# Performance work log

Measured on AMD Instinct MI355X. Metric: run time of the kernel, lower is better.

## Reference

```python
import jax, jax.numpy as jnp
import numpy as np

B, N, D, H = 8, 2048, 768, 64

def setup_inputs() -> dict:
    key = jax.random.key(0)
    k1, k2, k3, k4 = jax.random.split(key, 4)
    return {
        "input": jax.random.normal(k1, (B, N, D), dtype=jnp.float32),
        "Wq": jax.random.normal(k2, (D, H), dtype=jnp.float32) * (D ** -0.5),
        "Wk": jax.random.normal(k3, (D, H), dtype=jnp.float32) * (D ** -0.5),
        "Wv": jax.random.normal(k4, (D, H), dtype=jnp.float32) * (D ** -0.5),
    }

def reference(input, Wq, Wk, Wv):
    # Projections: [B, N, H]
    Q = jnp.einsum('bnd,dh->bnh', input, Wq)
    K = jnp.einsum('bnd,dh->bnh', input, Wk)
    V = jnp.einsum('bnd,dh->bnh', input, Wv)
    # Raw scores [B, N, N]; mask BEFORE scaling (as in original; -inf/scale == -inf)
    scores = jnp.einsum('bqh,bkh->bqk', Q, K)
    n = input.shape[1]
    causal = jnp.tril(jnp.ones((n, n), dtype=bool))
    scores = jnp.where(causal, scores, -jnp.inf)
    scores = scores / (K.shape[-1] ** 0.5)
    attn = jax.nn.softmax(scores, axis=-1)
    # dropout_rate=0 -> identity (eval mode)
    return jnp.einsum('bqk,bkh->bqh', attn, V)
```

## Files before the change

kernel.cpp:

```cpp
#include <hip/hip_runtime.h>
#include <stdint.h>

typedef __bf16 bf16_t;
typedef __bf16 bf16x8 __attribute__((ext_vector_type(8)));
typedef float floatx4 __attribute__((ext_vector_type(4)));

#define B_ 8
#define N_ 2048
#define D_ 768
#define H_ 64

__device__ __forceinline__ bf16_t f2bf(float f) {
    union { float f; uint32_t u; } v; v.f = f;
    uint32_t u = v.u;
    uint32_t r = (u + 0x7fffu + ((u >> 16) & 1u)) >> 16;
    union { unsigned short s; bf16_t b; } o; o.s = (unsigned short)r;
    return o.b;
}

__device__ __forceinline__ void async_cp16(void* l, const void* g) {
    __builtin_amdgcn_global_load_lds(
        (const __attribute__((address_space(1))) uint32_t*)g,
        (__attribute__((address_space(3))) uint32_t*)l, 16, 0, 0);
}

__global__ void wt_kernel(const float* __restrict__ Wq,
                          const float* __restrict__ Wk,
                          const float* __restrict__ Wv,
                          bf16_t* __restrict__ Wt) {
    const int h = threadIdx.x;
    const int k = blockIdx.x;
    const int s = blockIdx.y;
    const float* W = (s == 0) ? Wq : (s == 1) ? Wk : Wv;
    float v = W[k * H_ + h];
    if (s == 0) v *= 0.125f * 1.4426950408889634f;
    Wt[(size_t)(s * 64 + h) * D_ + k] = f2bf(v);
}

__launch_bounds__(256, 2)
__global__ void proj_kernel(const float* __restrict__ X,
                            const bf16_t* __restrict__ Wt,
                            bf16_t* __restrict__ Qb,
                            bf16_t* __restrict__ Kb,
                            bf16_t* __restrict__ Vt) {
    const int wave = threadIdx.x >> 6;
    const int lane = threadIdx.x & 63;
    const int quad = lane >> 4;
    const int l16  = lane & 15;
    const int rowhalf = wave & 1;
    const int colhalf = wave >> 1;
    const int m0blk = blockIdx.x * 32;

    __shared__ __align__(16) float  As[2][32 * 64];
    __shared__ __align__(16) bf16_t Bs[2][192 * 64];

    floatx4 acc[6];
#pragma unroll
    for (int i = 0; i < 6; i++) acc[i] = (floatx4){0.f, 0.f, 0.f, 0.f};

    auto stage = [&](int buf, int k0) {
#pragma unroll
        for (int i = 0; i < 2; i++) {
            const int r = (wave * 2 + i) * 4 + (lane >> 4);
            const int c = (lane & 15) ^ (r & 15);
            const float* g = X + (size_t)(m0blk + r) * D_ + k0 + c * 4;
            async_cp16((char*)&As[buf][0] + (wave * 2 + i) * 1024, g);
        }
#pragma unroll
        for (int i = 0; i < 6; i++) {
            const int r = (wave * 6 + i) * 8 + (lane >> 3);
            const int c = (lane & 7) ^ (r & 7);
            const bf16_t* g = Wt + (size_t)r * D_ + k0 + c * 8;
            async_cp16((char*)&Bs[buf][0] + (wave * 6 + i) * 1024, g);
        }
    };

    const int arow = rowhalf * 16 + l16;

    stage(0, 0);
    for (int ch = 0; ch < 12; ch++) {
        __syncthreads();
        if (ch + 1 < 12) stage((ch + 1) & 1, (ch + 1) * 64);

        const char* Ab = (const char*)&As[ch & 1][0];
        const char* Bb = (const char*)&Bs[ch & 1][0];
#pragma unroll
        for (int kh = 0; kh < 2; kh++) {
            const int c0 = kh * 8 + quad * 2;
            float4 xa = *(const float4*)(Ab + arow * 256 + ((c0 ^ l16) & 15) * 16);
            float4 xb = *(const float4*)(Ab + arow * 256 + (((c0 + 1) ^ l16) & 15) * 16);
            bf16x8 af;
            af[0] = f2bf(xa.x); af[1] = f2bf(xa.y);
            af[2] = f2bf(xa.z); af[3] = f2bf(xa.w);
            af[4] = f2bf(xb.x); af[5] = f2bf(xb.y);
            af[6] = f2bf(xb.z); af[7] = f2bf(xb.w);
            const int cb = kh * 4 + quad;
#pragma unroll
            for (int nt = 0; nt < 6; nt++) {
                const int n = colhalf * 96 + nt * 16 + l16;
                bf16x8 bf = *(const bf16x8*)(Bb + n * 128 + ((cb ^ (n & 7))) * 16);
                acc[nt] = __builtin_amdgcn_mfma_f32_16x16x32_bf16(af, bf, acc[nt], 0, 0, 0);
            }
        }
    }

#pragma unroll
    for (int nt = 0; nt < 6; nt++) {
        const int c = colhalf * 96 + nt * 16 + l16;
#pragma unroll
        for (int r = 0; r < 4; r++) {
            const int m = m0blk + rowhalf * 16 + quad * 4 + r;
            bf16_t val = f2bf(acc[nt][r]);
            if (c < 64) {
                Qb[(size_t)m * H_ + c] = val;
            } else if (c < 128) {
                Kb[(size_t)m * H_ + (c - 64)] = val;
            } else {
                const int b = m >> 11, n = m & 2047, h = c - 128;
                Vt[((size_t)b * H_ + h) * N_ + n] = val;
            }
        }
    }
}

__launch_bounds__(256, 4)
__global__ void attn_kernel(const bf16_t* __restrict__ Qb,
                            const bf16_t* __restrict__ Kb,
                            const bf16_t* __restrict__ Vt,
                            float* __restrict__ Out) {
    const int x = blockIdx.x;
    const int b = blockIdx.y;
    const int z = blockIdx.z;
    const int qt = z ? (127 - x) : x;
    const int q0 = qt * 16;

    const int wave = threadIdx.x >> 6;
    const int lane = threadIdx.x & 63;
    const int quad = lane >> 4;
    const int l16  = lane & 15;

    const bf16_t* Qp = Qb + ((size_t)b * N_ + q0) * H_;
    const bf16_t* Kp = Kb + (size_t)b * N_ * H_;
    const bf16_t* Vp = Vt + (size_t)b * H_ * N_;

    bf16x8 qf0 = *(const bf16x8*)(Qp + (size_t)l16 * H_ + quad * 8);
    bf16x8 qf1 = *(const bf16x8*)(Qp + (size_t)l16 * H_ + 32 + quad * 8);

    bf16x8 ones;
    {
        bf16_t one = f2bf(1.0f);
#pragma unroll
        for (int i = 0; i < 8; i++) ones[i] = one;
    }

    floatx4 o[4];
#pragma unroll
    for (int i = 0; i < 4; i++) o[i] = (floatx4){0.f, 0.f, 0.f, 0.f};
    floatx4 lsum = (floatx4){0.f, 0.f, 0.f, 0.f};

    __shared__ __align__(16) bf16_t Pl[4][16][32];
    __shared__ float Ol[3][16][64];
    __shared__ float Ll[3][16];

    const int kt_max = q0 >> 5;

    for (int kt = wave; kt <= kt_max; kt += 4) {
        const int k0 = kt << 5;

        const bf16_t* kp0 = Kp + (size_t)(k0 + l16) * H_ + quad * 8;
        const bf16_t* kp1 = kp0 + 16 * H_;
        bf16x8 kfa = *(const bf16x8*)kp0;
        bf16x8 kfb = *(const bf16x8*)(kp0 + 32);
        bf16x8 kfc = *(const bf16x8*)kp1;
        bf16x8 kfd = *(const bf16x8*)(kp1 + 32);
        const bf16_t* vp = Vp + (size_t)l16 * N_ + k0 + quad * 8;
        bf16x8 vf0 = *(const bf16x8*)(vp);
        bf16x8 vf1 = *(const bf16x8*)(vp + (size_t)16 * N_);
        bf16x8 vf2 = *(const bf16x8*)(vp + (size_t)32 * N_);
        bf16x8 vf3 = *(const bf16x8*)(vp + (size_t)48 * N_);

        floatx4 s0 = (floatx4){0.f, 0.f, 0.f, 0.f};
        floatx4 s1 = (floatx4){0.f, 0.f, 0.f, 0.f};
        s0 = __builtin_amdgcn_mfma_f32_16x16x32_bf16(qf0, kfa, s0, 0, 0, 0);
        s0 = __builtin_amdgcn_mfma_f32_16x16x32_bf16(qf1, kfb, s0, 0, 0, 0);
        s1 = __builtin_amdgcn_mfma_f32_16x16x32_bf16(qf0, kfc, s1, 0, 0, 0);
        s1 = __builtin_amdgcn_mfma_f32_16x16x32_bf16(qf1, kfd, s1, 0, 0, 0);

        float p[8];
        if (k0 + 31 <= q0) {
#pragma unroll
            for (int r = 0; r < 4; r++) {
                p[r]     = exp2f(s0[r]);
                p[4 + r] = exp2f(s1[r]);
            }
        } else {
            const int qrow = q0 + quad * 4;
#pragma unroll
            for (int r = 0; r < 4; r++) {
                p[r]     = (k0 + l16      <= qrow + r) ? exp2f(s0[r]) : 0.f;
                p[4 + r] = (k0 + 16 + l16 <= qrow + r) ? exp2f(s1[r]) : 0.f;
            }
        }

#pragma unroll
        for (int r = 0; r < 4; r++) {
            Pl[wave][quad * 4 + r][l16]      = f2bf(p[r]);
            Pl[wave][quad * 4 + r][16 + l16] = f2bf(p[4 + r]);
        }
        bf16x8 pf = *(const bf16x8*)(&Pl[wave][l16][quad * 8]);

        lsum = __builtin_amdgcn_mfma_f32_16x16x32_bf16(pf, ones, lsum, 0, 0, 0);
        o[0] = __builtin_amdgcn_mfma_f32_16x16x32_bf16(pf, vf0, o[0], 0, 0, 0);
        o[1] = __builtin_amdgcn_mfma_f32_16x16x32_bf16(pf, vf1, o[1], 0, 0, 0);
        o[2] = __builtin_amdgcn_mfma_f32_16x16x32_bf16(pf, vf2, o[2], 0, 0, 0);
        o[3] = __builtin_amdgcn_mfma_f32_16x16x32_bf16(pf, vf3, o[3], 0, 0, 0);
    }

    __syncthreads();
    if (wave != 0) {
#pragma unroll
        for (int nt = 0; nt < 4; nt++)
#pragma unroll
            for (int r = 0; r < 4; r++)
                Ol[wave - 1][quad * 4 + r][nt * 16 + l16] = o[nt][r];
        if (l16 == 0) {
#pragma unroll
            for (int r = 0; r < 4; r++)
                Ll[wave - 1][quad * 4 + r] = lsum[r];
        }
    }
    __syncthreads();
    if (wave == 0) {
#pragma unroll
        for (int r = 0; r < 4; r++) {
            const int row = quad * 4 + r;
            float l = lsum[r] + Ll[0][row] + Ll[1][row] + Ll[2][row];
            float inv = 1.0f / l;
#pragma unroll
            for (int nt = 0; nt < 4; nt++) {
                const int col = nt * 16 + l16;
                float v = o[nt][r] + Ol[0][row][col] + Ol[1][row][col] + Ol[2][row][col];
                Out[((size_t)b * N_ + q0 + row) * H_ + col] = v * inv;
            }
        }
    }
}

extern "C" void kernel_launch(void* const* d_in, const int* in_sizes, int n_in,
                              void* d_out, int out_size, void* d_ws, size_t ws_size,
                              hipStream_t stream) {
    const float* X  = (const float*)d_in[0];
    const float* Wq = (const float*)d_in[1];
    const float* Wk = (const float*)d_in[2];
    const float* Wv = (const float*)d_in[3];
    float* Out = (float*)d_out;

    char* ws = (char*)d_ws;
    bf16_t* Qb = (bf16_t*)(ws);
    bf16_t* Kb = (bf16_t*)(ws + (size_t)(2u << 20));
    bf16_t* Vt = (bf16_t*)(ws + (size_t)(4u << 20));
    bf16_t* Wt = (bf16_t*)(ws + (size_t)(6u << 20));

    hipLaunchKernelGGL(wt_kernel, dim3(768, 3), dim3(64), 0, stream, Wq, Wk, Wv, Wt);
    hipLaunchKernelGGL(proj_kernel, dim3(512), dim3(256), 0, stream, X, Wt, Qb, Kb, Vt);
    hipLaunchKernelGGL(attn_kernel, dim3(64, 8, 2), dim3(256), 0, stream, Qb, Kb, Vt, Out);
}
```

Before: 133.1 us.

## Double-buffer K/V tiles in LDS via async global-to-LDS loads per wave

Each wave now prefetches its K and V tiles into a private double-buffered LDS region using async global_load_lds copies with an XOR swizzle. Manual waitcnt and sched_barriers overlap the next tile's load with the current tile's MFMA work, replacing direct register loads from global memory. The P scratch buffer gets a padded row stride, and the output-reduction buffers alias the staging memory. LDS use grows to about 72KB per block, so launch bounds drop to 2 blocks per SM and occupancy is reduced.

```diff
diff --git a/kernel.cpp b/kernel.cpp
--- a/kernel.cpp
+++ b/kernel.cpp
@@ -9,6 +9,10 @@
 #define N_ 2048
 #define D_ 768
 #define H_ 64
+
+#define WAIT_VM8()   { __builtin_amdgcn_sched_barrier(0); __builtin_amdgcn_s_waitcnt(0x0F78); __builtin_amdgcn_sched_barrier(0); }
+#define WAIT_VM0()   { __builtin_amdgcn_sched_barrier(0); __builtin_amdgcn_s_waitcnt(0x0F70); __builtin_amdgcn_sched_barrier(0); }
+#define WAIT_LGKM0() { __builtin_amdgcn_sched_barrier(0); __builtin_amdgcn_s_waitcnt(0xC07F); __builtin_amdgcn_sched_barrier(0); }
 
 __device__ __forceinline__ bf16_t f2bf(float f) {
     union { float f; uint32_t u; } v; v.f = f;
@@ -123,7 +127,7 @@
     }
 }
 
-__launch_bounds__(256, 4)
+__launch_bounds__(256, 2)
 __global__ void attn_kernel(const bf16_t* __restrict__ Qb,
                             const bf16_t* __restrict__ Kb,
                             const bf16_t* __restrict__ Vt,
@@ -139,9 +143,15 @@
     const int quad = lane >> 4;
     const int l16  = lane & 15;
 
+    __shared__ __align__(16) char smem[4 * 16384 + 4 * 16 * 56 * 2];
+    char* stg = smem;
+    bf16_t* Pl = (bf16_t*)(smem + 65536);
+    float* Ol  = (float*)smem;
+    float* Ll  = (float*)(smem + 12288);
+
     const bf16_t* Qp = Qb + ((size_t)b * N_ + q0) * H_;
-    const bf16_t* Kp = Kb + (size_t)b * N_ * H_;
-    const bf16_t* Vp = Vt + (size_t)b * H_ * N_;
+    const char* Kp = (const char*)(Kb + (size_t)b * N_ * H_);
+    const char* Vp = (const char*)(Vt + (size_t)b * H_ * N_);
 
     bf16x8 qf0 = *(const bf16x8*)(Qp + (size_t)l16 * H_ + quad * 8);
     bf16x8 qf1 = *(const bf16x8*)(Qp + (size_t)l16 * H_ + 32 + quad * 8);
@@ -158,26 +168,50 @@
     for (int i = 0; i < 4; i++) o[i] = (floatx4){0.f, 0.f, 0.f, 0.f};
     floatx4 lsum = (floatx4){0.f, 0.f, 0.f, 0.f};
 
-    __shared__ __align__(16) bf16_t Pl[4][16][32];
-    __shared__ float Ol[3][16][64];
-    __shared__ float Ll[3][16];
-
-    const int kt_max = q0 >> 5;
-
-    for (int kt = wave; kt <= kt_max; kt += 4) {
+    char* mybase = stg + wave * 16384;
+
+    const int rK = lane >> 3, cK = lane & 7;
+    const int rV = lane >> 2, cV = lane & 3;
+    auto stage_kv = [&](int k0, char* buf) {
+#pragma unroll
+        for (int i = 0; i < 4; i++) {
+            const int r = i * 8 + rK;
+            const char* g = Kp + (size_t)(k0 + r) * 128 + (cK ^ (r & 7)) * 16;
+            async_cp16(buf + i * 1024, g);
+        }
+#pragma unroll
+        for (int i = 0; i < 4; i++) {
+            const int r = i * 16 + rV;
+            const char* g = Vp + (size_t)r * 4096 + (size_t)k0 * 2 + (cV ^ (r & 3)) * 16;
+            async_cp16(buf + 4096 + i * 1024, g);
+        }
+    };
+
+    const int ktm = q0 >> 5;
+
+    if (wave <= ktm)     stage_kv(wave << 5,       mybase);
+    if (wave + 4 <= ktm) stage_kv((wave + 4) << 5, mybase + 8192);
+
+    for (int kt = wave; kt <= ktm; kt += 4) {
         const int k0 = kt << 5;
-
-        const bf16_t* kp0 = Kp + (size_t)(k0 + l16) * H_ + quad * 8;
-        const bf16_t* kp1 = kp0 + 16 * H_;
-        bf16x8 kfa = *(const bf16x8*)kp0;
-        bf16x8 kfb = *(const bf16x8*)(kp0 + 32);
-        bf16x8 kfc = *(const bf16x8*)kp1;
-        bf16x8 kfd = *(const bf16x8*)(kp1 + 32);
-        const bf16_t* vp = Vp + (size_t)l16 * N_ + k0 + quad * 8;
-        bf16x8 vf0 = *(const bf16x8*)(vp);
-        bf16x8 vf1 = *(const bf16x8*)(vp + (size_t)16 * N_);
-        bf16x8 vf2 = *(const bf16x8*)(vp + (size_t)32 * N_);
-        bf16x8 vf3 = *(const bf16x8*)(vp + (size_t)48 * N_);
+        const int buf = (((kt - wave) >> 2) & 1);
+        const char* kb = mybase + buf * 8192;
+        const char* vb = kb + 4096;
+
+        if (kt + 4 <= ktm) { WAIT_VM8(); } else { WAIT_VM0(); }
+
+        const int krow = l16 * 128;
+        bf16x8 kfa = *(const bf16x8*)(kb + krow        + ((quad    ) ^ (l16 & 7)) * 16);
+        bf16x8 kfb = *(const bf16x8*)(kb + krow        + ((quad + 4) ^ (l16 & 7)) * 16);
+        bf16x8 kfc = *(const bf16x8*)(kb + krow + 2048 + ((quad    ) ^ (l16 & 7)) * 16);
+        bf16x8 kfd = *(const bf16x8*)(kb + krow + 2048 + ((quad + 4) ^ (l16 & 7)) * 16);
+        bf16x8 vf0 = *(const bf16x8*)(vb + (l16     ) * 64 + (quad ^ (l16 & 3)) * 16);
+        bf16x8 vf1 = *(const bf16x8*)(vb + (l16 + 16) * 64 + (quad ^ (l16 & 3)) * 16);
+        bf16x8 vf2 = *(const bf16x8*)(vb + (l16 + 32) * 64 + (quad ^ (l16 & 3)) * 16);
+        bf16x8 vf3 = *(const bf16x8*)(vb + (l16 + 48) * 64 + (quad ^ (l16 & 3)) * 16);
+
+        WAIT_LGKM0();
+        if (kt + 8 <= ktm) stage_kv((kt + 8) << 5, mybase + buf * 8192);
 
         floatx4 s0 = (floatx4){0.f, 0.f, 0.f, 0.f};
         floatx4 s1 = (floatx4){0.f, 0.f, 0.f, 0.f};
@@ -202,12 +236,13 @@
             }
         }
 
+        bf16_t* Pw = Pl + wave * 16 * 56;
 #pragma unroll
         for (int r = 0; r < 4; r++) {
-            Pl[wave][quad * 4 + r][l16]      = f2bf(p[r]);
-            Pl[wave][quad * 4 + r][16 + l16] = f2bf(p[4 + r]);
-        }
-        bf16x8 pf = *(const bf16x8*)(&Pl[wave][l16][quad * 8]);
+            Pw[(quad * 4 + r) * 56 + l16]      = f2bf(p[r]);
+            Pw[(quad * 4 + r) * 56 + 16 + l16] = f2bf(p[4 + r]);
+        }
+        bf16x8 pf = *(const bf16x8*)(Pw + l16 * 56 + quad * 8);
 
         lsum = __builtin_amdgcn_mfma_f32_16x16x32_bf16(pf, ones, lsum, 0, 0, 0);
         o[0] = __builtin_amdgcn_mfma_f32_16x16x32_bf16(pf, vf0, o[0], 0, 0, 0);
@@ -218,15 +253,16 @@
 
     __syncthreads();
     if (wave != 0) {
+        float* Ow = Ol + (wave - 1) * 16 * 64;
 #pragma unroll
         for (int nt = 0; nt < 4; nt++)
 #pragma unroll
             for (int r = 0; r < 4; r++)
-                Ol[wave - 1][quad * 4 + r][nt * 16 + l16] = o[nt][r];
+                Ow[(quad * 4 + r) * 64 + nt * 16 + l16] = o[nt][r];
         if (l16 == 0) {
 #pragma unroll
             for (int r = 0; r < 4; r++)
-                Ll[wave - 1][quad * 4 + r] = lsum[r];
+                Ll[(wave - 1) * 16 + quad * 4 + r] = lsum[r];
         }
     }
     __syncthreads();
@@ -234,12 +270,13 @@
 #pragma unroll
         for (int r = 0; r < 4; r++) {
             const int row = quad * 4 + r;
-            float l = lsum[r] + Ll[0][row] + Ll[1][row] + Ll[2][row];
+            float l = lsum[r] + Ll[row] + Ll[16 + row] + Ll[32 + row];
             float inv = 1.0f / l;
 #pragma unroll
             for (int nt = 0; nt < 4; nt++) {
                 const int col = nt * 16 + l16;
-                float v = o[nt][r] + Ol[0][row][col] + Ol[1][row][col] + Ol[2][row][col];
+                float v = o[nt][r] + Ol[row * 64 + col]
+                        + Ol[(16 + row) * 64 + col] + Ol[(32 + row) * 64 + col];
                 Out[((size_t)b * N_ + q0 + row) * H_ + col] = v * inv;
             }
         }
```

Measured after the change: 126.1 us. -5.2%, faster.

## Restructure attention kernel to 32-row query tiles with async double-buffered LDS K/V staging

Applied to the files above, without the earlier changes.

The attention kernel now handles 32 query rows per block using 32x32x16 MFMAs, which halves the grid and doubles K/V reuse per load. Each wave streams K and V tiles into its own swizzled LDS double buffer through async global-to-LDS copies, with explicit waitcnt barriers, so loads overlap compute. The row sum is now accumulated in registers instead of through an MFMA against a ones vector. In exchange it uses more LDS and registers (launch bounds drop to 2) and has fewer blocks, which may hurt occupancy and load balance.

```diff
diff --git a/kernel.cpp b/kernel.cpp
--- a/kernel.cpp
+++ b/kernel.cpp
@@ -2,13 +2,19 @@
 #include <stdint.h>
 
 typedef __bf16 bf16_t;
+typedef __bf16 bf16x4 __attribute__((ext_vector_type(4)));
 typedef __bf16 bf16x8 __attribute__((ext_vector_type(8)));
 typedef float floatx4 __attribute__((ext_vector_type(4)));
+typedef float floatx16 __attribute__((ext_vector_type(16)));
 
 #define B_ 8
 #define N_ 2048
 #define D_ 768
 #define H_ 64
+
+#define WAIT_VM8()   { __builtin_amdgcn_sched_barrier(0); __builtin_amdgcn_s_waitcnt(0x0F78); __builtin_amdgcn_sched_barrier(0); }
+#define WAIT_VM0()   { __builtin_amdgcn_sched_barrier(0); __builtin_amdgcn_s_waitcnt(0x0F70); __builtin_amdgcn_sched_barrier(0); }
+#define WAIT_LGKM0() { __builtin_amdgcn_sched_barrier(0); __builtin_amdgcn_s_waitcnt(0xC07F); __builtin_amdgcn_sched_barrier(0); }
 
 __device__ __forceinline__ bf16_t f2bf(float f) {
     union { float f; uint32_t u; } v; v.f = f;
@@ -123,7 +129,7 @@
     }
 }
 
-__launch_bounds__(256, 4)
+__launch_bounds__(256, 2)
 __global__ void attn_kernel(const bf16_t* __restrict__ Qb,
                             const bf16_t* __restrict__ Kb,
                             const bf16_t* __restrict__ Vt,
@@ -131,117 +137,150 @@
     const int x = blockIdx.x;
     const int b = blockIdx.y;
     const int z = blockIdx.z;
-    const int qt = z ? (127 - x) : x;
-    const int q0 = qt * 16;
+    const int qt = z ? (63 - x) : x;
+    const int q0 = qt * 32;
 
     const int wave = threadIdx.x >> 6;
     const int lane = threadIdx.x & 63;
-    const int quad = lane >> 4;
-    const int l16  = lane & 15;
-
-    const bf16_t* Qp = Qb + ((size_t)b * N_ + q0) * H_;
-    const bf16_t* Kp = Kb + (size_t)b * N_ * H_;
-    const bf16_t* Vp = Vt + (size_t)b * H_ * N_;
-
-    bf16x8 qf0 = *(const bf16x8*)(Qp + (size_t)l16 * H_ + quad * 8);
-    bf16x8 qf1 = *(const bf16x8*)(Qp + (size_t)l16 * H_ + 32 + quad * 8);
-
-    bf16x8 ones;
-    {
-        bf16_t one = f2bf(1.0f);
-#pragma unroll
-        for (int i = 0; i < 8; i++) ones[i] = one;
-    }
-
-    floatx4 o[4];
-#pragma unroll
-    for (int i = 0; i < 4; i++) o[i] = (floatx4){0.f, 0.f, 0.f, 0.f};
-    floatx4 lsum = (floatx4){0.f, 0.f, 0.f, 0.f};
-
-    __shared__ __align__(16) bf16_t Pl[4][16][32];
-    __shared__ float Ol[3][16][64];
-    __shared__ float Ll[3][16];
-
-    const int kt_max = q0 >> 5;
-
-    for (int kt = wave; kt <= kt_max; kt += 4) {
-        const int k0 = kt << 5;
-
-        const bf16_t* kp0 = Kp + (size_t)(k0 + l16) * H_ + quad * 8;
-        const bf16_t* kp1 = kp0 + 16 * H_;
-        bf16x8 kfa = *(const bf16x8*)kp0;
-        bf16x8 kfb = *(const bf16x8*)(kp0 + 32);
-        bf16x8 kfc = *(const bf16x8*)kp1;
-        bf16x8 kfd = *(const bf16x8*)(kp1 + 32);
-        const bf16_t* vp = Vp + (size_t)l16 * N_ + k0 + quad * 8;
-        bf16x8 vf0 = *(const bf16x8*)(vp);
-        bf16x8 vf1 = *(const bf16x8*)(vp + (size_t)16 * N_);
-        bf16x8 vf2 = *(const bf16x8*)(vp + (size_t)32 * N_);
-        bf16x8 vf3 = *(const bf16x8*)(vp + (size_t)48 * N_);
-
-        floatx4 s0 = (floatx4){0.f, 0.f, 0.f, 0.f};
-        floatx4 s1 = (floatx4){0.f, 0.f, 0.f, 0.f};
-        s0 = __builtin_amdgcn_mfma_f32_16x16x32_bf16(qf0, kfa, s0, 0, 0, 0);
-        s0 = __builtin_amdgcn_mfma_f32_16x16x32_bf16(qf1, kfb, s0, 0, 0, 0);
-        s1 = __builtin_amdgcn_mfma_f32_16x16x32_bf16(qf0, kfc, s1, 0, 0, 0);
-        s1 = __builtin_amdgcn_mfma_f32_16x16x32_bf16(qf1, kfd, s1, 0, 0, 0);
-
-        float p[8];
-        if (k0 + 31 <= q0) {
-#pragma unroll
-            for (int r = 0; r < 4; r++) {
-                p[r]     = exp2f(s0[r]);
-                p[4 + r] = exp2f(s1[r]);
+    const int hi   = lane >> 5;
+    const int lq   = lane & 31;
+
+    __shared__ __align__(16) char smem[4 * 16384 + 4 * 2048];
+    char* mybase = smem + wave * 16384;
+    char* Pimg   = smem + 65536 + wave * 2048;
+    float* Ol = (float*)smem;
+    float* Ll = (float*)(smem + 24576);
+
+    const bf16_t* qrow = Qb + ((size_t)b * N_ + q0 + lq) * H_ + hi * 8;
+    bf16x8 qf0 = *(const bf16x8*)(qrow);
+    bf16x8 qf1 = *(const bf16x8*)(qrow + 16);
+    bf16x8 qf2 = *(const bf16x8*)(qrow + 32);
+    bf16x8 qf3 = *(const bf16x8*)(qrow + 48);
+
+    floatx16 o0, o1;
+#pragma unroll
+    for (int i = 0; i < 16; i++) { o0[i] = 0.f; o1[i] = 0.f; }
+    float ls = 0.f;
+
+    const bf16_t* KpB = Kb + (size_t)b * N_ * H_;
+    const bf16_t* VpB = Vt + (size_t)b * H_ * N_;
+
+    const int rK = lane >> 3, cK = lane & 7;
+    const int rV = lane >> 2, cV = lane & 3;
+    const int mVl = (rV & 3) ^ ((rV & 4) >> 2);
+    auto stage_kv = [&](int k0, char* buf) {
+#pragma unroll
+        for (int i = 0; i < 4; i++) {
+            const int r = i * 8 + rK;
+            const int mk = rK ^ (((i & 1) << 2));
+            async_cp16(buf + i * 1024,
+                       KpB + (size_t)(k0 + r) * H_ + (cK ^ mk) * 8);
+        }
+#pragma unroll
+        for (int i = 0; i < 4; i++) {
+            const int h = i * 16 + rV;
+            async_cp16(buf + 4096 + i * 1024,
+                       VpB + (size_t)h * N_ + k0 + (cV ^ mVl) * 8);
+        }
+    };
+
+    const int ktm = qt;
+    if (wave <= ktm)     stage_kv(wave * 32, mybase);
+    if (wave + 4 <= ktm) stage_kv((wave + 4) * 32, mybase + 8192);
+
+    const int mK = (lq & 7) ^ ((lq & 8) >> 1);
+    const int m8 = (lq & 7) ^ ((lq & 8) >> 1);
+
+    for (int kt = wave; kt <= ktm; kt += 4) {
+        const int k0 = kt * 32;
+        char* kb = mybase + (((((kt - wave) >> 2) & 1)) ? 8192 : 0);
+        char* vb = kb + 4096;
+
+        if (kt + 4 <= ktm) { WAIT_VM8(); } else { WAIT_VM0(); }
+
+        bf16x8 kf0 = *(const bf16x8*)(kb + lq * 128 + (((0 + hi) ^ mK) * 16));
+        bf16x8 kf1 = *(const bf16x8*)(kb + lq * 128 + (((2 + hi) ^ mK) * 16));
+        bf16x8 kf2 = *(const bf16x8*)(kb + lq * 128 + (((4 + hi) ^ mK) * 16));
+        bf16x8 kf3 = *(const bf16x8*)(kb + lq * 128 + (((6 + hi) ^ mK) * 16));
+        const int mV0 = (lq & 3) ^ ((lq & 4) >> 2);
+        bf16x8 vf00 = *(const bf16x8*)(vb + (lq     ) * 64 + (((0 + hi) ^ mV0) * 16));
+        bf16x8 vf01 = *(const bf16x8*)(vb + (lq     ) * 64 + (((2 + hi) ^ mV0) * 16));
+        bf16x8 vf10 = *(const bf16x8*)(vb + (lq + 32) * 64 + (((0 + hi) ^ mV0) * 16));
+        bf16x8 vf11 = *(const bf16x8*)(vb + (lq + 32) * 64 + (((2 + hi) ^ mV0) * 16));
+
+        WAIT_LGKM0();
+        if (kt + 8 <= ktm) stage_kv(k0 + 256, kb);
+
+        floatx16 st;
+#pragma unroll
+        for (int i = 0; i < 16; i++) st[i] = 0.f;
+        st = __builtin_amdgcn_mfma_f32_32x32x16_bf16(kf0, qf0, st, 0, 0, 0);
+        st = __builtin_amdgcn_mfma_f32_32x32x16_bf16(kf1, qf1, st, 0, 0, 0);
+        st = __builtin_amdgcn_mfma_f32_32x32x16_bf16(kf2, qf2, st, 0, 0, 0);
+        st = __builtin_amdgcn_mfma_f32_32x32x16_bf16(kf3, qf3, st, 0, 0, 0);
+
+        float p[16];
+        if (kt < qt) {
+#pragma unroll
+            for (int r = 0; r < 16; r++) p[r] = exp2f(st[r]);
+        } else {
+#pragma unroll
+            for (int r = 0; r < 16; r++) {
+                const int row = (r & 3) + 8 * (r >> 2) + 4 * hi;
+                p[r] = (row <= lq) ? exp2f(st[r]) : 0.f;
             }
-        } else {
-            const int qrow = q0 + quad * 4;
-#pragma unroll
-            for (int r = 0; r < 4; r++) {
-                p[r]     = (k0 + l16      <= qrow + r) ? exp2f(s0[r]) : 0.f;
-                p[4 + r] = (k0 + 16 + l16 <= qrow + r) ? exp2f(s1[r]) : 0.f;
-            }
-        }
-
-#pragma unroll
-        for (int r = 0; r < 4; r++) {
-            Pl[wave][quad * 4 + r][l16]      = f2bf(p[r]);
-            Pl[wave][quad * 4 + r][16 + l16] = f2bf(p[4 + r]);
-        }
-        bf16x8 pf = *(const bf16x8*)(&Pl[wave][l16][quad * 8]);
-
-        lsum = __builtin_amdgcn_mfma_f32_16x16x32_bf16(pf, ones, lsum, 0, 0, 0);
-        o[0] = __builtin_amdgcn_mfma_f32_16x16x32_bf16(pf, vf0, o[0], 0, 0, 0);
-        o[1] = __builtin_amdgcn_mfma_f32_16x16x32_bf16(pf, vf1, o[1], 0, 0, 0);
-        o[2] = __builtin_amdgcn_mfma_f32_16x16x32_bf16(pf, vf2, o[2], 0, 0, 0);
-        o[3] = __builtin_amdgcn_mfma_f32_16x16x32_bf16(pf, vf3, o[3], 0, 0, 0);
-    }
-
+        }
+#pragma unroll
+        for (int r = 0; r < 16; r++) ls += p[r];
+
+#pragma unroll
+        for (int g = 0; g < 4; g++) {
+            bf16x4 w;
+            w[0] = f2bf(p[g * 4 + 0]); w[1] = f2bf(p[g * 4 + 1]);
+            w[2] = f2bf(p[g * 4 + 2]); w[3] = f2bf(p[g * 4 + 3]);
+            const int sub = g * 2 + hi;
+            *(bf16x4*)(Pimg + lq * 64 + ((sub ^ m8) * 8)) = w;
+        }
+
+#pragma unroll
+        for (int s2 = 0; s2 < 2; s2++) {
+            const int sub0 = s2 * 4 + hi * 2;
+            bf16x4 a0 = *(const bf16x4*)(Pimg + lq * 64 + (((sub0    ) ^ m8) * 8));
+            bf16x4 a1 = *(const bf16x4*)(Pimg + lq * 64 + (((sub0 + 1) ^ m8) * 8));
+            bf16x8 pf;
+            pf[0] = a0[0]; pf[1] = a0[1]; pf[2] = a0[2]; pf[3] = a0[3];
+            pf[4] = a1[0]; pf[5] = a1[1]; pf[6] = a1[2]; pf[7] = a1[3];
+            o0 = __builtin_amdgcn_mfma_f32_32x32x16_bf16(pf, (s2 ? vf01 : vf00), o0, 0, 0, 0);
+            o1 = __builtin_amdgcn_mfma_f32_32x32x16_bf16(pf, (s2 ? vf11 : vf10), o1, 0, 0, 0);
+        }
+    }
+
+    float lst = ls + __shfl_xor(ls, 32, 64);
     __syncthreads();
+    if (hi == 0) Ll[wave * 32 + lq] = lst;
     if (wave != 0) {
-#pragma unroll
-        for (int nt = 0; nt < 4; nt++)
-#pragma unroll
-            for (int r = 0; r < 4; r++)
-                Ol[wave - 1][quad * 4 + r][nt * 16 + l16] = o[nt][r];
-        if (l16 == 0) {
-#pragma unroll
-            for (int r = 0; r < 4; r++)
-                Ll[wave - 1][quad * 4 + r] = lsum[r];
+        float* Ow = Ol + (wave - 1) * 2048;
+#pragma unroll
+        for (int r = 0; r < 16; r++) {
+            const int q = (r & 3) + 8 * (r >> 2) + 4 * hi;
+            Ow[q * 64 + lq]      = o0[r];
+            Ow[q * 64 + 32 + lq] = o1[r];
         }
     }
     __syncthreads();
     if (wave == 0) {
 #pragma unroll
-        for (int r = 0; r < 4; r++) {
-            const int row = quad * 4 + r;
-            float l = lsum[r] + Ll[0][row] + Ll[1][row] + Ll[2][row];
-            float inv = 1.0f / l;
-#pragma unroll
-            for (int nt = 0; nt < 4; nt++) {
-                const int col = nt * 16 + l16;
-                float v = o[nt][r] + Ol[0][row][col] + Ol[1][row][col] + Ol[2][row][col];
-                Out[((size_t)b * N_ + q0 + row) * H_ + col] = v * inv;
-            }
+        for (int r = 0; r < 16; r++) {
+            const int q = (r & 3) + 8 * (r >> 2) + 4 * hi;
+            const float l4 = Ll[q] + Ll[32 + q] + Ll[64 + q] + Ll[96 + q];
+            const float inv = 1.0f / l4;
+            float v0 = o0[r] + Ol[q * 64 + lq]
+                     + Ol[2048 + q * 64 + lq] + Ol[4096 + q * 64 + lq];
+            float v1 = o1[r] + Ol[q * 64 + 32 + lq]
+                     + Ol[2048 + q * 64 + 32 + lq] + Ol[4096 + q * 64 + 32 + lq];
+            const size_t base = ((size_t)b * N_ + q0 + q) * H_;
+            Out[base + lq]      = v0 * inv;
+            Out[base + 32 + lq] = v1 * inv;
         }
     }
 }
@@ -263,5 +302,5 @@
 
     hipLaunchKernelGGL(wt_kernel, dim3(768, 3), dim3(64), 0, stream, Wq, Wk, Wv, Wt);
     hipLaunchKernelGGL(proj_kernel, dim3(512), dim3(256), 0, stream, X, Wt, Qb, Kb, Vt);
-    hipLaunchKernelGGL(attn_kernel, dim3(64, 8, 2), dim3(256), 0, stream, Qb, Kb, Vt, Out);
-}
+    hipLaunchKernelGGL(attn_kernel, dim3(32, 8, 2), dim3(256), 0, stream, Qb, Kb, Vt, Out);
+}
```

Measured after the change: 120.9 us. 9.1% less time.
